# Kernel optimization log

Hardware: AMD Instinct MI355X
Metric: run time of the kernel (lower is better)

The kernel has to match this reference:

```python
import jax, jax.numpy as jnp
import numpy as np

T, B = 128, 4096          # rollout length, num parallel envs
H = 128                   # lstm hidden
FEAT = 96                 # 32 (image) + 32 (loc) + 32 (energy)
NA = 6                    # num_actions
GRID, MAXE = 10.0, 200.0


def setup_inputs() -> dict:
    key = jax.random.key(0)
    ks = jax.random.split(key, 24)
    N = T * B
    w = lambda k, shp, s=0.05: (jax.random.normal(k, shp, jnp.float32) * s)
    return {
        "image": jax.random.uniform(ks[0], (N, 5, 5), jnp.float32),
        "location": jax.random.uniform(ks[1], (N, 2), jnp.float32),
        "energy": jax.random.uniform(ks[2], (N, 1), jnp.float32),
        "done": jax.random.randint(ks[3], (N,), 0, 2).astype(jnp.int32),
        "h0": jnp.zeros((B, H), jnp.float32),
        "c0": jnp.zeros((B, H), jnp.float32),
        # visual encoder MLP 25->256->256->128->32
        "W1": w(ks[4], (25, 256)),  "b1": jnp.zeros(256, jnp.float32),
        "W2": w(ks[5], (256, 256)), "b2": jnp.zeros(256, jnp.float32),
        "W3": w(ks[6], (256, 128)), "b3": jnp.zeros(128, jnp.float32),
        "W4": w(ks[7], (128, 32)),  "b4": jnp.zeros(32, jnp.float32),
        # location / energy encoders
        "Wl": w(ks[8], (2, 32)), "bl": jnp.zeros(32, jnp.float32),
        "We": w(ks[9], (1, 32)), "be": jnp.zeros(32, jnp.float32),
        # LSTM (PyTorch layout: gates [i,f,g,o], W_ih: [4H, in], W_hh: [4H, H])
        "Wih": w(ks[10], (4 * H, FEAT)), "Whh": w(ks[11], (4 * H, H)),
        "bih": jnp.zeros(4 * H, jnp.float32), "bhh": jnp.zeros(4 * H, jnp.float32),
        # actor / critic heads
        "Wa": w(ks[12], (H, NA)), "ba": jnp.zeros(NA, jnp.float32),
        "Wc": w(ks[13], (H, 1)),  "bc": jnp.zeros(1, jnp.float32),
    }


def _forward(image, location, energy, done, h0, c0,
             W1, b1, W2, b2, W3, b3, W4, b4, Wl, bl, We, be,
             Wih, Whh, bih, bhh, Wa, ba, Wc, bc):
    relu = jax.nn.relu
    x = image.reshape(-1, 25) / 255.0                      # [N,25]
    f = relu(x @ W1 + b1)
    f = relu(f @ W2 + b2)
    f = relu(f @ W3 + b3)
    img_feat = relu(f @ W4 + b4)                           # [N,32]
    loc_feat = (location / GRID) @ Wl + bl                 # [N,32]
    eng_feat = (energy / MAXE) @ We + be                   # [N,32]
    feats = jnp.concatenate([img_feat, loc_feat, eng_feat], axis=1)  # [N,96]
    xs = feats.reshape(T, B, FEAT)
    ds = done.astype(jnp.float32).reshape(T, B)
    bias = bih + bhh                                       # [4H]

    def step(carry, inp):
        h, c = carry                                       # [B,H]
        x_t, d_t = inp
        mask = (1.0 - d_t)[:, None]                        # reset on done
        h = h * mask
        c = c * mask
        gates = x_t @ Wih.T + h @ Whh.T + bias             # [B,4H]
        i, fg, g, o = jnp.split(gates, 4, axis=1)
        c = jax.nn.sigmoid(fg) * c + jax.nn.sigmoid(i) * jnp.tanh(g)
        h = jax.nn.sigmoid(o) * jnp.tanh(c)
        return (h, c), h

    (hT, cT), hs = jax.lax.scan(step, (h0, c0), (xs, ds))  # hs: [T,B,H]
    hidden = hs.reshape(-1, H)                             # [N,H]
    logits = hidden @ Wa + ba                              # [N,NA]
    value = hidden @ Wc + bc                               # [N,1]
    return jnp.concatenate([logits, value], axis=1)        # [N,NA+1]


def reference(image, location, energy, done, h0, c0,
              W1, b1, W2, b2, W3, b3, W4, b4, Wl, bl, We, be,
              Wih, Whh, bih, bhh, Wa, ba, Wc, bc):
    return _forward(image, location, energy, done, h0, c0,
                    W1, b1, W2, b2, W3, b3, W4, b4, Wl, bl, We, be,
                    Wih, Whh, bih, bhh, Wa, ba, Wc, bc)
```

## Files before the change

kernel.cpp:

```cpp
#include <hip/hip_runtime.h>

#define T_ 128
#define B_ 4096
#define N_ (T_*B_)
#define H_ 128
#define FEAT_ 96
#define K_ 224
#define G4H_ 512

typedef __attribute__((ext_vector_type(8))) short short8;
typedef __attribute__((ext_vector_type(4))) short short4v;
typedef __attribute__((ext_vector_type(4))) float f32x4;

__device__ __forceinline__ float fsig(float x) {
    float e = __builtin_amdgcn_exp2f(-1.44269504088896340736f * x);
    return __builtin_amdgcn_rcpf(1.0f + e);
}
__device__ __forceinline__ float ftanh(float x) {
    float e = __builtin_amdgcn_exp2f(-2.88539008177792681472f * x);
    return fmaf(2.0f, __builtin_amdgcn_rcpf(1.0f + e), -1.0f);
}
__device__ __forceinline__ short f2bf(float f) {
    unsigned u = __builtin_bit_cast(unsigned, f);
    u += 0x7fff + ((u >> 16) & 1);
    return (short)(u >> 16);
}
__device__ __forceinline__ short4v pack4relu(const f32x4 a) {
    short4v v;
    v[0] = f2bf(fmaxf(a[0], 0.f)); v[1] = f2bf(fmaxf(a[1], 0.f));
    v[2] = f2bf(fmaxf(a[2], 0.f)); v[3] = f2bf(fmaxf(a[3], 0.f));
    return v;
}

#define FBASE(t, grp, kk) ((((size_t)(t) * 256 + (grp)) * 3 + (kk)) * 512)

__global__ __launch_bounds__(256) void prep_kernel(
    const float* __restrict__ Wih, const float* __restrict__ Whh,
    const float* __restrict__ bih, const float* __restrict__ bhh,
    const float* __restrict__ W1, const float* __restrict__ W2,
    const float* __restrict__ W3, const float* __restrict__ W4,
    short* __restrict__ Wtp, float* __restrict__ bias,
    short* __restrict__ W1p, short* __restrict__ W2p,
    short* __restrict__ W3p, short* __restrict__ W4p)
{
    int idx = blockIdx.x * 256 + threadIdx.x;
    if (idx < 114688) {
        int j = idx & 7, L = (idx >> 3) & 63, r = idx >> 9;
        int kk = r % 7, n = r / 7;
        int k = kk * 32 + ((L >> 4) << 3) + j;
        int g = (n << 4) + (L & 15);
        float v = (k < FEAT_) ? Wih[g * FEAT_ + k] : Whh[g * H_ + (k - FEAT_)];
        Wtp[idx] = f2bf(v);
        return;
    }
    int e = idx - 114688;
    if (e < 8192) {
        int j = e & 7, L = (e >> 3) & 63, nt = e >> 9;
        int k = ((L >> 4) << 3) + j;
        int o = nt * 16 + (L & 15);
        W1p[e] = (k < 25) ? f2bf(W1[k * 256 + o]) : (short)0;
        return;
    }
    e -= 8192;
    if (e < 65536) {
        int j = e & 7, L = (e >> 3) & 63, f = e >> 9;
        int kk = f & 7, nt = f >> 3;
        int k = kk * 32 + ((L >> 4) << 3) + j;
        W2p[e] = f2bf(W2[k * 256 + nt * 16 + (L & 15)]);
        return;
    }
    e -= 65536;
    if (e < 32768) {
        int j = e & 7, L = (e >> 3) & 63, f = e >> 9;
        int kk = f & 7, nt = f >> 3;
        int k = kk * 32 + ((L >> 4) << 3) + j;
        W3p[e] = f2bf(W3[k * 128 + nt * 16 + (L & 15)]);
        return;
    }
    e -= 32768;
    if (e < 4096) {
        int j = e & 7, L = (e >> 3) & 63, f = e >> 9;
        int kk = f & 3, nt = f >> 2;
        int k = kk * 32 + ((L >> 4) << 3) + j;
        W4p[e] = f2bf(W4[k * 32 + nt * 16 + (L & 15)]);
        return;
    }
    e -= 4096;
    if (e < 512) bias[e] = bih[e] + bhh[e];
}

__global__ __launch_bounds__(256) void loc_kernel(
    const float* __restrict__ location, const float* __restrict__ energy,
    const float* __restrict__ Wl, const float* __restrict__ bl,
    const float* __restrict__ We, const float* __restrict__ be,
    short* __restrict__ featsb)
{
    __shared__ float C[160];
    const int tid = threadIdx.x;
    if (tid < 160) {
        float v;
        if (tid < 64)       v = Wl[tid];
        else if (tid < 96)  v = bl[tid - 64];
        else if (tid < 128) v = We[tid - 96];
        else                v = be[tid - 128];
        C[tid] = v;
    }
    __syncthreads();
    const int n = blockIdx.x * 64 + (tid >> 2);
    const int p = tid & 3;
    const float lx = location[(size_t)n * 2 + 0] * 0.1f;
    const float ly = location[(size_t)n * 2 + 1] * 0.1f;
    const float ev = energy[n] * (1.0f / 200.0f);
    const int t = n >> 12, b = n & 4095;
    const int grp = b >> 4, bi = b & 15;
    const int kk = 1 + (p >> 1);
    #pragma unroll
    for (int o = 0; o < 2; o++) {
        const int f0 = 32 + p * 16 + o * 8;
        short8 v;
        #pragma unroll
        for (int j = 0; j < 8; j++) {
            const int f = f0 + j;
            float val;
            if (f < 64) { const int cix = f - 32; val = fmaf(lx, C[cix], fmaf(ly, C[32 + cix], C[64 + cix])); }
            else        { const int cix = f - 64; val = fmaf(ev, C[96 + cix], C[128 + cix]); }
            v[j] = f2bf(val);
        }
        const int Lhi = ((p & 1) << 1) + o;
        *(short8*)&featsb[FBASE(t, grp, kk) + (Lhi * 16 + bi) * 8] = v;
    }
}

__global__ __launch_bounds__(512, 2) void enc_kernel(
    const float* __restrict__ image,
    const short* __restrict__ W1p, const float* __restrict__ b1,
    const short* __restrict__ W2p, const float* __restrict__ b2,
    const short* __restrict__ W3p, const float* __restrict__ b3,
    const short* __restrict__ W4p, const float* __restrict__ b4,
    short* __restrict__ featsb)
{
    __shared__ float Raw[2][800];
    __shared__ __align__(16) short In[2 * 512];
    __shared__ __align__(16) short AA[2 * 8 * 512];
    __shared__ __align__(16) short AB[2 * 8 * 512];
    const int tid  = threadIdx.x;
    const int lane = tid & 63, wv = tid >> 6;
    const int col  = lane & 15, quad = lane >> 4;

    short8 w1r[2], w2r[2][8], w3r[8], w4r[4];
    #pragma unroll
    for (int i = 0; i < 2; i++)
        w1r[i] = *(const short8*)&W1p[((wv + 8 * i) * 64 + lane) * 8];
    #pragma unroll
    for (int i = 0; i < 2; i++)
        #pragma unroll
        for (int kk = 0; kk < 8; kk++)
            w2r[i][kk] = *(const short8*)&W2p[(((wv + 8 * i) * 8 + kk) * 64 + lane) * 8];
    #pragma unroll
    for (int kk = 0; kk < 8; kk++)
        w3r[kk] = *(const short8*)&W3p[((wv * 8 + kk) * 64 + lane) * 8];
    #pragma unroll
    for (int kk = 0; kk < 4; kk++)
        w4r[kk] = *(const short8*)&W4p[(((wv & 1) * 4 + kk) * 64 + lane) * 8];
    float4 b1r[2], b2r[2];
    #pragma unroll
    for (int i = 0; i < 2; i++) {
        b1r[i] = *(const float4*)(b1 + (wv + 8 * i) * 16 + quad * 4);
        b2r[i] = *(const float4*)(b2 + (wv + 8 * i) * 16 + quad * 4);
    }
    const float4 b3r = *(const float4*)(b3 + wv * 16 + quad * 4);
    const float4 b4r = *(const float4*)(b4 + (wv & 1) * 16 + quad * 4);

    const bool ld = tid < 400;
    float2 ir = {0.f, 0.f};
    int tile = blockIdx.x;
    if (ld) {
        float2 t0 = *(const float2*)(image + (size_t)tile * 800 + 2 * tid);
        Raw[0][2 * tid] = t0.x; Raw[0][2 * tid + 1] = t0.y;
        ir = *(const float2*)(image + (size_t)(tile + 256) * 800 + 2 * tid);
    }
    __syncthreads();

    for (int it = 0; it < 64; it++) {
        const int cur = it & 1, nxt = cur ^ 1;
        tile = it * 256 + blockIdx.x;
        if (tid < 128) {
            const int st = tid >> 6, L = tid & 63;
            const int s = st * 16 + (L & 15), kb = (L >> 4) * 8;
            short8 v;
            #pragma unroll
            for (int j = 0; j < 8; j++) {
                const int kx = kb + j;
                v[j] = (kx < 25) ? f2bf(Raw[cur][s * 25 + kx] * (1.0f / 255.0f)) : (short)0;
            }
            *(short8*)&In[(st * 64 + L) * 8] = v;
        }
        if (ld && it + 1 < 64) { Raw[nxt][2 * tid] = ir.x; Raw[nxt][2 * tid + 1] = ir.y; }
        if (ld && it + 2 < 64)
            ir = *(const float2*)(image + (size_t)(tile + 512) * 800 + 2 * tid);
        __syncthreads();

        {
            short8 bx[2];
            #pragma unroll
            for (int st = 0; st < 2; st++) bx[st] = *(const short8*)&In[(st * 64 + lane) * 8];
            #pragma unroll
            for (int i = 0; i < 2; i++) {
                const int nt = wv + 8 * i;
                #pragma unroll
                for (int st = 0; st < 2; st++) {
                    f32x4 acc = (f32x4){b1r[i].x, b1r[i].y, b1r[i].z, b1r[i].w};
                    acc = __builtin_amdgcn_mfma_f32_16x16x32_bf16(w1r[i], bx[st], acc, 0, 0, 0);
                    *(short4v*)&AA[((st * 8 + (nt >> 1)) * 64 + ((((nt & 1) << 1) + (quad >> 1)) << 4) + col) * 8 + (quad & 1) * 4]
                        = pack4relu(acc);
                }
            }
        }
        __syncthreads();

        {
            f32x4 acc[2][2];
            #pragma unroll
            for (int i = 0; i < 2; i++)
                #pragma unroll
                for (int st = 0; st < 2; st++)
                    acc[i][st] = (f32x4){b2r[i].x, b2r[i].y, b2r[i].z, b2r[i].w};
            #pragma unroll
            for (int kk = 0; kk < 8; kk++) {
                short8 bx[2];
                #pragma unroll
                for (int st = 0; st < 2; st++)
                    bx[st] = *(const short8*)&AA[((st * 8 + kk) * 64 + lane) * 8];
                #pragma unroll
                for (int i = 0; i < 2; i++)
                    #pragma unroll
                    for (int st = 0; st < 2; st++)
                        acc[i][st] = __builtin_amdgcn_mfma_f32_16x16x32_bf16(w2r[i][kk], bx[st], acc[i][st], 0, 0, 0);
            }
            #pragma unroll
            for (int i = 0; i < 2; i++) {
                const int nt = wv + 8 * i;
                #pragma unroll
                for (int st = 0; st < 2; st++)
                    *(short4v*)&AB[((st * 8 + (nt >> 1)) * 64 + ((((nt & 1) << 1) + (quad >> 1)) << 4) + col) * 8 + (quad & 1) * 4]
                        = pack4relu(acc[i][st]);
            }
        }
        __syncthreads();

        {
            f32x4 acc[2];
            #pragma unroll
            for (int st = 0; st < 2; st++) acc[st] = (f32x4){b3r.x, b3r.y, b3r.z, b3r.w};
            #pragma unroll
            for (int kk = 0; kk < 8; kk++) {
                #pragma unroll
                for (int st = 0; st < 2; st++) {
                    const short8 bx = *(const short8*)&AB[((st * 8 + kk) * 64 + lane) * 8];
                    acc[st] = __builtin_amdgcn_mfma_f32_16x16x32_bf16(w3r[kk], bx, acc[st], 0, 0, 0);
                }
            }
            const int nt = wv;
            #pragma unroll
            for (int st = 0; st < 2; st++)
                *(short4v*)&AA[((st * 8 + (nt >> 1)) * 64 + ((((nt & 1) << 1) + (quad >> 1)) << 4) + col) * 8 + (quad & 1) * 4]
                    = pack4relu(acc[st]);
        }
        __syncthreads();

        if (wv < 4) {
            const int nt = wv & 1, st = wv >> 1;
            f32x4 acc = (f32x4){b4r.x, b4r.y, b4r.z, b4r.w};
            #pragma unroll
            for (int kk = 0; kk < 4; kk++) {
                const short8 bx = *(const short8*)&AA[((st * 8 + kk) * 64 + lane) * 8];
                acc = __builtin_amdgcn_mfma_f32_16x16x32_bf16(w4r[kk], bx, acc, 0, 0, 0);
            }
            const int t4 = tile >> 7;
            const int grp = (tile & 127) * 2 + st;
            *(short4v*)&featsb[FBASE(t4, grp, 0) + (((nt << 1) + (quad >> 1)) * 16 + col) * 8 + (quad & 1) * 4]
                = pack4relu(acc);
        }
        __syncthreads();
    }
}

__global__ __launch_bounds__(512, 2) void lstm_kernel(
    const short* __restrict__ featsb, const int* __restrict__ done,
    const float* __restrict__ h0, const float* __restrict__ c0,
    const short* __restrict__ Wtp, const float* __restrict__ bias,
    const float* __restrict__ Wa, const float* __restrict__ ba,
    const float* __restrict__ Wc, const float* __restrict__ bc,
    float* __restrict__ out)
{
    __shared__ __align__(16) short Hb[2][4 * 64 * 8];
    __shared__ __align__(16) short HW[4 * 64 * 8];
    __shared__ float Ml[T_ * 16];

    const int tid = threadIdx.x;
    const int r0 = blockIdx.x * 16;
    const int grp = r0 >> 4;
    const int lane = tid & 63;
    const int wv = tid >> 6;
    const int col = lane & 15;
    const int quad = lane >> 4;
    const int u = (wv << 4) + col;

    short8 wtr[4][7];
    #pragma unroll
    for (int g = 0; g < 4; g++)
        #pragma unroll
        for (int kk = 0; kk < 7; kk++)
            wtr[g][kk] = *(const short8*)&Wtp[((size_t)((wv + 8 * g) * 7 + kk) * 64 + lane) * 8];

    for (int idx = tid; idx < 4 * 64 * 8; idx += 512) {
        int j = idx & 7, L = (idx >> 3) & 63, kk2 = idx >> 9;
        int k = kk2 * 32 + ((L >> 4) << 3) + j;
        int n = L & 15;
        float v = (n < 6) ? Wa[k * 6 + n] : (n == 6 ? Wc[k] : 0.0f);
        HW[idx] = f2bf(v);
    }
    for (int idx = tid; idx < T_ * 16; idx += 512)
        Ml[idx] = 1.0f - (float)done[(size_t)(idx >> 4) * B_ + r0 + (idx & 15)];

    const int kk2h = wv >> 1;
    const int Lhi_h = ((wv & 1) << 1) | (col >> 3);
    const int jh = col & 7;
    f32x4 c;
    #pragma unroll
    for (int r = 0; r < 4; r++) {
        const int s = (quad << 2) + r;
        const float m = 1.0f - (float)done[r0 + s];
        c[r] = c0[(size_t)(r0 + s) * H_ + u] * m;
        Hb[0][(kk2h * 64 + Lhi_h * 16 + s) * 8 + jh] = f2bf(h0[(size_t)(r0 + s) * H_ + u]);
    }
    const float bi0 = bias[((wv +  0) << 4) + col];
    const float bi1 = bias[((wv +  8) << 4) + col];
    const float bi2 = bias[((wv + 16) << 4) + col];
    const float bi3 = bias[((wv + 24) << 4) + col];
    const float hb = (col < 6) ? ba[col] : (col == 6 ? bc[0] : 0.0f);

    short8 xa[3], xb[3];
    #pragma unroll
    for (int kk = 0; kk < 3; kk++) {
        xa[kk] = *(const short8*)&featsb[FBASE(0, grp, kk) + lane * 8];
        xb[kk] = *(const short8*)&featsb[FBASE(1, grp, kk) + lane * 8];
    }
    __syncthreads();

    for (int t = 0; t < T_; t++) {
        const int cur = t & 1, nxt = cur ^ 1;
        const float mcol = Ml[t * 16 + col];
        f32x4 acc0 = {bi0, bi0, bi0, bi0};
        f32x4 acc1 = {bi1, bi1, bi1, bi1};
        f32x4 acc2 = {bi2, bi2, bi2, bi2};
        f32x4 acc3 = {bi3, bi3, bi3, bi3};
        #pragma unroll
        for (int kk = 0; kk < 7; kk++) {
            short8 af;
            if (kk < 3) af = xa[kk];
            else {
                af = *(const short8*)&Hb[cur][((kk - 3) * 64 + lane) * 8];
                if (mcol == 0.0f) af = (short8){0,0,0,0,0,0,0,0};
            }
            acc0 = __builtin_amdgcn_mfma_f32_16x16x32_bf16(af, wtr[0][kk], acc0, 0, 0, 0);
            acc1 = __builtin_amdgcn_mfma_f32_16x16x32_bf16(af, wtr[1][kk], acc1, 0, 0, 0);
            acc2 = __builtin_amdgcn_mfma_f32_16x16x32_bf16(af, wtr[2][kk], acc2, 0, 0, 0);
            acc3 = __builtin_amdgcn_mfma_f32_16x16x32_bf16(af, wtr[3][kk], acc3, 0, 0, 0);
        }
        float4 mn = {1.f, 1.f, 1.f, 1.f};
        if (t < T_ - 1) mn = *(const float4*)&Ml[(t + 1) * 16 + (quad << 2)];
        #pragma unroll
        for (int r = 0; r < 4; r++) {
            const float ig = fsig(acc0[r]);
            const float fg = fsig(acc1[r]);
            const float gg = ftanh(acc2[r]);
            const float og = fsig(acc3[r]);
            const float cn = fmaf(fg, c[r], ig * gg);
            const float h = og * ftanh(cn);
            c[r] = cn * ((&mn.x)[r]);
            Hb[nxt][(kk2h * 64 + Lhi_h * 16 + (quad << 2) + r) * 8 + jh] = f2bf(h);
        }
        #pragma unroll
        for (int kk = 0; kk < 3; kk++) xa[kk] = xb[kk];
        if (t + 2 < T_) {
            #pragma unroll
            for (int kk = 0; kk < 3; kk++)
                xb[kk] = *(const short8*)&featsb[FBASE(t + 2, grp, kk) + lane * 8];
        }
        __syncthreads();

        if (wv == 0) {
            f32x4 ha = {hb, hb, hb, hb};
            #pragma unroll
            for (int kk2 = 0; kk2 < 4; kk2++) {
                const short8 hf = *(const short8*)&Hb[nxt][(kk2 * 64 + lane) * 8];
                const short8 wf = *(const short8*)&HW[(kk2 * 64 + lane) * 8];
                ha = __builtin_amdgcn_mfma_f32_16x16x32_bf16(hf, wf, ha, 0, 0, 0);
            }
            if (col < 7) {
                #pragma unroll
                for (int r = 0; r < 4; r++) {
                    const int s = (quad << 2) + r;
                    out[((size_t)t * B_ + r0 + s) * 7 + col] = ha[r];
                }
            }
        }
    }
}

extern "C" void kernel_launch(void* const* d_in, const int* in_sizes, int n_in,
                              void* d_out, int out_size, void* d_ws, size_t ws_size,
                              hipStream_t stream) {
    const float* image    = (const float*)d_in[0];
    const float* location = (const float*)d_in[1];
    const float* energy   = (const float*)d_in[2];
    const int*   done     = (const int*)d_in[3];
    const float* h0       = (const float*)d_in[4];
    const float* c0       = (const float*)d_in[5];
    const float* W1 = (const float*)d_in[6];   const float* b1 = (const float*)d_in[7];
    const float* W2 = (const float*)d_in[8];   const float* b2 = (const float*)d_in[9];
    const float* W3 = (const float*)d_in[10];  const float* b3 = (const float*)d_in[11];
    const float* W4 = (const float*)d_in[12];  const float* b4 = (const float*)d_in[13];
    const float* Wl = (const float*)d_in[14];  const float* bl = (const float*)d_in[15];
    const float* We = (const float*)d_in[16];  const float* be = (const float*)d_in[17];
    const float* Wih = (const float*)d_in[18]; const float* Whh = (const float*)d_in[19];
    const float* bih = (const float*)d_in[20]; const float* bhh = (const float*)d_in[21];
    const float* Wa = (const float*)d_in[22];  const float* ba = (const float*)d_in[23];
    const float* Wc = (const float*)d_in[24];  const float* bc = (const float*)d_in[25];

    char* ws = (char*)d_ws;
    short* Wtp   = (short*)ws;
    float* bias  = (float*)(ws + 229376);
    short* W1p   = (short*)(ws + 231424);
    short* W2p   = (short*)(ws + 247808);
    short* W3p   = (short*)(ws + 378880);
    short* W4p   = (short*)(ws + 444416);
    short* featsb = (short*)(ws + 452608);
    float* out   = (float*)d_out;

    prep_kernel<<<882, 256, 0, stream>>>(Wih, Whh, bih, bhh, W1, W2, W3, W4,
                                         Wtp, bias, W1p, W2p, W3p, W4p);
    loc_kernel<<<N_ / 64, 256, 0, stream>>>(location, energy, Wl, bl, We, be, featsb);
    enc_kernel<<<256, 512, 0, stream>>>(image, W1p, b1, W2p, b2, W3p, b3, W4p, b4, featsb);
    lstm_kernel<<<B_ / 16, 512, 0, stream>>>(featsb, done, h0, c0, Wtp, bias,
                                             Wa, ba, Wc, bc, out);
}
```

Baseline: 445.5 us.

## Fold activation scales into weights, pipeline encoder input prep, rotate head wave

Prescales the LSTM gate weights and biases by log2(e), or by 2*log2(e) for the g gate, so sigmoid and tanh no longer need a multiply before exp2. It also folds the 1/255 image scale into W1. In the encoder, idle waves convert the next tile's raw input during layer 4, which removes one barrier per iteration, and layer 3 output gets its own LDS buffer. The LSTM loop is unrolled by two so the xa/xb register copy goes away, and the actor/critic head work rotates across waves instead of always landing on wave 0. The risks are extra bf16 rounding from prescaled weights and race hazards from the removed barrier.

```diff
diff --git a/kernel.cpp b/kernel.cpp
--- a/kernel.cpp
+++ b/kernel.cpp
@@ -7,17 +7,17 @@
 #define FEAT_ 96
 #define K_ 224
 #define G4H_ 512
+#define L2E 1.4426950408889634f
 
 typedef __attribute__((ext_vector_type(8))) short short8;
 typedef __attribute__((ext_vector_type(4))) short short4v;
 typedef __attribute__((ext_vector_type(4))) float f32x4;
 
-__device__ __forceinline__ float fsig(float x) {
-    float e = __builtin_amdgcn_exp2f(-1.44269504088896340736f * x);
-    return __builtin_amdgcn_rcpf(1.0f + e);
+__device__ __forceinline__ float sig2(float x) {
+    return __builtin_amdgcn_rcpf(1.0f + __builtin_amdgcn_exp2f(-x));
 }
 __device__ __forceinline__ float ftanh(float x) {
-    float e = __builtin_amdgcn_exp2f(-2.88539008177792681472f * x);
+    float e = __builtin_amdgcn_exp2f(-2.0f * L2E * x);
     return fmaf(2.0f, __builtin_amdgcn_rcpf(1.0f + e), -1.0f);
 }
 __device__ __forceinline__ short f2bf(float f) {
@@ -50,7 +50,8 @@
         int k = kk * 32 + ((L >> 4) << 3) + j;
         int g = (n << 4) + (L & 15);
         float v = (k < FEAT_) ? Wih[g * FEAT_ + k] : Whh[g * H_ + (k - FEAT_)];
-        Wtp[idx] = f2bf(v);
+        float s = (n >= 16 && n < 24) ? (2.0f * L2E) : L2E;
+        Wtp[idx] = f2bf(v * s);
         return;
     }
     int e = idx - 114688;
@@ -58,7 +59,7 @@
         int j = e & 7, L = (e >> 3) & 63, nt = e >> 9;
         int k = ((L >> 4) << 3) + j;
         int o = nt * 16 + (L & 15);
-        W1p[e] = (k < 25) ? f2bf(W1[k * 256 + o]) : (short)0;
+        W1p[e] = (k < 25) ? f2bf(W1[k * 256 + o] * (1.0f / 255.0f)) : (short)0;
         return;
     }
     e -= 8192;
@@ -86,7 +87,10 @@
         return;
     }
     e -= 4096;
-    if (e < 512) bias[e] = bih[e] + bhh[e];
+    if (e < 512) {
+        float s = ((e >> 7) == 2) ? (2.0f * L2E) : L2E;
+        bias[e] = (bih[e] + bhh[e]) * s;
+    }
 }
 
 __global__ __launch_bounds__(256) void loc_kernel(
@@ -143,6 +147,7 @@
     __shared__ __align__(16) short In[2 * 512];
     __shared__ __align__(16) short AA[2 * 8 * 512];
     __shared__ __align__(16) short AB[2 * 8 * 512];
+    __shared__ __align__(16) short AC[2 * 4 * 512];
     const int tid  = threadIdx.x;
     const int lane = tid & 63, wv = tid >> 6;
     const int col  = lane & 15, quad = lane >> 4;
@@ -172,29 +177,30 @@
     const float4 b4r = *(const float4*)(b4 + (wv & 1) * 16 + quad * 4);
 
     const bool ld = tid < 400;
+    const int w4t = tid - 256;
     float2 ir = {0.f, 0.f};
-    int tile = blockIdx.x;
+
     if (ld) {
-        float2 t0 = *(const float2*)(image + (size_t)tile * 800 + 2 * tid);
+        float2 t0 = *(const float2*)(image + (size_t)blockIdx.x * 800 + 2 * tid);
         Raw[0][2 * tid] = t0.x; Raw[0][2 * tid + 1] = t0.y;
-        ir = *(const float2*)(image + (size_t)(tile + 256) * 800 + 2 * tid);
+        ir = *(const float2*)(image + (size_t)(blockIdx.x + 256) * 800 + 2 * tid);
     }
     __syncthreads();
+    if (w4t >= 0 && w4t < 128) {
+        const int st = w4t >> 6, L = w4t & 63;
+        const int s = st * 16 + (L & 15), kb = (L >> 4) * 8;
+        short8 v;
+        #pragma unroll
+        for (int j = 0; j < 8; j++) {
+            const int kx = kb + j;
+            v[j] = (kx < 25) ? f2bf(Raw[0][s * 25 + kx]) : (short)0;
+        }
+        *(short8*)&In[(st * 64 + L) * 8] = v;
+    }
 
     for (int it = 0; it < 64; it++) {
-        const int cur = it & 1, nxt = cur ^ 1;
-        tile = it * 256 + blockIdx.x;
-        if (tid < 128) {
-            const int st = tid >> 6, L = tid & 63;
-            const int s = st * 16 + (L & 15), kb = (L >> 4) * 8;
-            short8 v;
-            #pragma unroll
-            for (int j = 0; j < 8; j++) {
-                const int kx = kb + j;
-                v[j] = (kx < 25) ? f2bf(Raw[cur][s * 25 + kx] * (1.0f / 255.0f)) : (short)0;
-            }
-            *(short8*)&In[(st * 64 + L) * 8] = v;
-        }
+        const int nxt = (it & 1) ^ 1;
+        const int tile = it * 256 + blockIdx.x;
         if (ld && it + 1 < 64) { Raw[nxt][2 * tid] = ir.x; Raw[nxt][2 * tid + 1] = ir.y; }
         if (ld && it + 2 < 64)
             ir = *(const float2*)(image + (size_t)(tile + 512) * 800 + 2 * tid);
@@ -263,7 +269,7 @@
             const int nt = wv;
             #pragma unroll
             for (int st = 0; st < 2; st++)
-                *(short4v*)&AA[((st * 8 + (nt >> 1)) * 64 + ((((nt & 1) << 1) + (quad >> 1)) << 4) + col) * 8 + (quad & 1) * 4]
+                *(short4v*)&AC[((st * 4 + (nt >> 1)) * 64 + ((((nt & 1) << 1) + (quad >> 1)) << 4) + col) * 8 + (quad & 1) * 4]
                     = pack4relu(acc[st]);
         }
         __syncthreads();
@@ -273,15 +279,24 @@
             f32x4 acc = (f32x4){b4r.x, b4r.y, b4r.z, b4r.w};
             #pragma unroll
             for (int kk = 0; kk < 4; kk++) {
-                const short8 bx = *(const short8*)&AA[((st * 8 + kk) * 64 + lane) * 8];
+                const short8 bx = *(const short8*)&AC[((st * 4 + kk) * 64 + lane) * 8];
                 acc = __builtin_amdgcn_mfma_f32_16x16x32_bf16(w4r[kk], bx, acc, 0, 0, 0);
             }
             const int t4 = tile >> 7;
             const int grp = (tile & 127) * 2 + st;
             *(short4v*)&featsb[FBASE(t4, grp, 0) + (((nt << 1) + (quad >> 1)) * 16 + col) * 8 + (quad & 1) * 4]
                 = pack4relu(acc);
-        }
-        __syncthreads();
+        } else if (w4t >= 0 && w4t < 128 && it + 1 < 64) {
+            const int st = w4t >> 6, L = w4t & 63;
+            const int s = st * 16 + (L & 15), kb = (L >> 4) * 8;
+            short8 v;
+            #pragma unroll
+            for (int j = 0; j < 8; j++) {
+                const int kx = kb + j;
+                v[j] = (kx < 25) ? f2bf(Raw[nxt][s * 25 + kx]) : (short)0;
+            }
+            *(short8*)&In[(st * 64 + L) * 8] = v;
+        }
     }
 }
 
@@ -348,8 +363,8 @@
     }
     __syncthreads();
 
-    for (int t = 0; t < T_; t++) {
-        const int cur = t & 1, nxt = cur ^ 1;
+    auto STEP = [&](int t, int cur, short8* X) {
+        const int nxt = cur ^ 1;
         const float mcol = Ml[t * 16 + col];
         f32x4 acc0 = {bi0, bi0, bi0, bi0};
         f32x4 acc1 = {bi1, bi1, bi1, bi1};
@@ -358,7 +373,7 @@
         #pragma unroll
         for (int kk = 0; kk < 7; kk++) {
             short8 af;
-            if (kk < 3) af = xa[kk];
+            if (kk < 3) af = X[kk];
             else {
                 af = *(const short8*)&Hb[cur][((kk - 3) * 64 + lane) * 8];
                 if (mcol == 0.0f) af = (short8){0,0,0,0,0,0,0,0};
@@ -372,25 +387,23 @@
         if (t < T_ - 1) mn = *(const float4*)&Ml[(t + 1) * 16 + (quad << 2)];
         #pragma unroll
         for (int r = 0; r < 4; r++) {
-            const float ig = fsig(acc0[r]);
-            const float fg = fsig(acc1[r]);
-            const float gg = ftanh(acc2[r]);
-            const float og = fsig(acc3[r]);
-            const float cn = fmaf(fg, c[r], ig * gg);
+            const float ig = sig2(acc0[r]);
+            const float fg = sig2(acc1[r]);
+            const float gt = fmaf(2.0f, sig2(acc2[r]), -1.0f);
+            const float og = sig2(acc3[r]);
+            const float cn = fmaf(fg, c[r], ig * gt);
             const float h = og * ftanh(cn);
             c[r] = cn * ((&mn.x)[r]);
             Hb[nxt][(kk2h * 64 + Lhi_h * 16 + (quad << 2) + r) * 8 + jh] = f2bf(h);
         }
-        #pragma unroll
-        for (int kk = 0; kk < 3; kk++) xa[kk] = xb[kk];
         if (t + 2 < T_) {
             #pragma unroll
             for (int kk = 0; kk < 3; kk++)
-                xb[kk] = *(const short8*)&featsb[FBASE(t + 2, grp, kk) + lane * 8];
+                X[kk] = *(const short8*)&featsb[FBASE(t + 2, grp, kk) + lane * 8];
         }
         __syncthreads();
 
-        if (wv == 0) {
+        if (wv == (t & 7)) {
             f32x4 ha = {hb, hb, hb, hb};
             #pragma unroll
             for (int kk2 = 0; kk2 < 4; kk2++) {
@@ -406,6 +419,11 @@
                 }
             }
         }
+    };
+
+    for (int t = 0; t < T_; t += 2) {
+        STEP(t, 0, xa);
+        STEP(t + 1, 1, xb);
     }
 }
 
```

Result: faster. 427.6 us (-4.0%).
